# Kernel optimization log

Measured on AMD Instinct MI355X. Metric: run time of the kernel, lower is better.

Reference implementation:

```python
import jax, jax.numpy as jnp
import numpy as np

B, T, C, H = 16, 2048, 1024, 64

def setup_inputs() -> dict:
    key = jax.random.key(0)
    kx, kq, kk, kv = jax.random.split(key, 4)
    x = jax.random.normal(kx, (B, T, C), dtype=jnp.float32)
    Wq = jax.random.normal(kq, (C, H), dtype=jnp.float32) * (C ** -0.5)
    Wk = jax.random.normal(kk, (C, H), dtype=jnp.float32) * (C ** -0.5)
    Wv = jax.random.normal(kv, (C, H), dtype=jnp.float32) * (C ** -0.5)
    return {"x": x, "Wq": Wq, "Wk": Wk, "Wv": Wv}

def reference(x, Wq, Wk, Wv):
    # q,k,v: [B,T,H]
    q = jnp.einsum('btc,ch->bth', x, Wq)
    k = jnp.einsum('btc,ch->bth', x, Wk)
    v = jnp.einsum('btc,ch->bth', x, Wv)
    scale = k.shape[-1] ** -0.5
    # scores: [B,T,T], causal mask then softmax (dropout=0 -> identity)
    w = jnp.einsum('bth,bsh->bts', q, k) * scale
    causal = jnp.tril(jnp.ones((x.shape[1], x.shape[1]), dtype=bool))
    w = jnp.where(causal[None, :, :], w, -jnp.inf)
    w = jax.nn.softmax(w, axis=-1)
    out = jnp.einsum('bts,bsh->bth', w, v)
    return out
```

## Files before the change

kernel.cpp:

```cpp
#include <hip/hip_runtime.h>


#define B_ 16
#define T_ 2048
#define C_ 1024
#define H_ 64
#define QK_ELEMS (B_ * T_ * H_)

typedef float  f32x4  __attribute__((ext_vector_type(4)));
typedef __bf16 bf16x8 __attribute__((ext_vector_type(8)));
typedef __bf16 bf16x4 __attribute__((ext_vector_type(4)));

__global__ __launch_bounds__(256) void wt_kernel(const float* __restrict__ Wq,
                                                 const float* __restrict__ Wk,
                                                 const float* __restrict__ Wv,
                                                 __bf16* __restrict__ Wt) {
    __shared__ float tl[64][65];
    const int mat = blockIdx.x >> 4;
    const int c0  = (blockIdx.x & 15) * 64;
    const float* W = (mat == 0) ? Wq : (mat == 1) ? Wk : Wv;
    const int t  = threadIdx.x;
    const int r4 = t >> 6;
    const int cc = t & 63;
#pragma unroll
    for (int i = 0; i < 16; i++) {
        const int c = r4 + i * 4;
        tl[c][cc] = W[(size_t)(c0 + c) * H_ + cc];
    }
    __syncthreads();
#pragma unroll
    for (int i = 0; i < 16; i++) {
        const int h = r4 + i * 4;
        Wt[(size_t)mat * 65536 + (size_t)h * C_ + c0 + cc] = (__bf16)tl[cc][h];
    }
}

__global__ __launch_bounds__(256) void qkv_kernel(const float* __restrict__ x,
                                                  const __bf16* __restrict__ Wt,
                                                  __bf16* __restrict__ Qw,
                                                  __bf16* __restrict__ Kw,
                                                  __bf16* __restrict__ Vtw) {
    __shared__ __align__(16) __bf16 Alds[2][64 * 72];
    __shared__ __align__(16) __bf16 Blds[2][192 * 72];

    const int tid  = threadIdx.x;
    const int w    = tid >> 6;
    const int lane = tid & 63;
    const int quad = lane >> 4;
    const int l15  = lane & 15;
    const int wm   = (w & 1) * 32;
    const int wn   = (w >> 1) * 96;
    const int m0   = blockIdx.x * 64;

    f32x4 acc[12];
#pragma unroll
    for (int i = 0; i < 12; i++) acc[i] = (f32x4){0.f, 0.f, 0.f, 0.f};

    const int ar = tid >> 3;
    const int ac = (tid & 7) * 8;
    const float* xA = x + (size_t)(m0 + ar) * C_ + ac;
    const __bf16* wB = Wt + (size_t)ar * C_ + ac;

    float4 a0, a1, a2, a3;
    bf16x8 br[6];

    auto loadA = [&](int k0) {
        a0 = *(const float4*)(xA + k0);
        a1 = *(const float4*)(xA + k0 + 4);
        a2 = *(const float4*)(xA + k0 + 32 * C_);
        a3 = *(const float4*)(xA + k0 + 32 * C_ + 4);
    };
    auto loadB = [&](int k0) {
#pragma unroll
        for (int i = 0; i < 6; i++)
            br[i] = *(const bf16x8*)(wB + (size_t)i * 32 * C_ + k0);
    };
    auto storeLds = [&](int buf) {
        bf16x8 v0, v1;
        v0[0]=(__bf16)a0.x; v0[1]=(__bf16)a0.y; v0[2]=(__bf16)a0.z; v0[3]=(__bf16)a0.w;
        v0[4]=(__bf16)a1.x; v0[5]=(__bf16)a1.y; v0[6]=(__bf16)a1.z; v0[7]=(__bf16)a1.w;
        v1[0]=(__bf16)a2.x; v1[1]=(__bf16)a2.y; v1[2]=(__bf16)a2.z; v1[3]=(__bf16)a2.w;
        v1[4]=(__bf16)a3.x; v1[5]=(__bf16)a3.y; v1[6]=(__bf16)a3.z; v1[7]=(__bf16)a3.w;
        *(bf16x8*)&Alds[buf][ar * 72 + ac]        = v0;
        *(bf16x8*)&Alds[buf][(ar + 32) * 72 + ac] = v1;
#pragma unroll
        for (int i = 0; i < 6; i++)
            *(bf16x8*)&Blds[buf][(ar + i * 32) * 72 + ac] = br[i];
    };

    loadA(0); loadB(0); storeLds(0);

    for (int k = 0; k < 16; k++) {
        __syncthreads();
        if (k < 15) { loadA((k + 1) * 64); loadB((k + 1) * 64); }
        const int buf = k & 1;
#pragma unroll
        for (int kh = 0; kh < 2; kh++) {
            bf16x8 af0 = *(const bf16x8*)&Alds[buf][(wm + l15) * 72 + kh * 32 + quad * 8];
            bf16x8 af1 = *(const bf16x8*)&Alds[buf][(wm + 16 + l15) * 72 + kh * 32 + quad * 8];
#pragma unroll
            for (int nt = 0; nt < 6; nt++) {
                bf16x8 bf = *(const bf16x8*)&Blds[buf][(wn + nt * 16 + l15) * 72 + kh * 32 + quad * 8];
                acc[nt]     = __builtin_amdgcn_mfma_f32_16x16x32_bf16(af0, bf, acc[nt], 0, 0, 0);
                acc[6 + nt] = __builtin_amdgcn_mfma_f32_16x16x32_bf16(af1, bf, acc[6 + nt], 0, 0, 0);
            }
        }
        if (k < 15) storeLds((k + 1) & 1);
    }

#pragma unroll
    for (int mt = 0; mt < 2; mt++) {
        const int row0 = m0 + wm + mt * 16 + quad * 4;
#pragma unroll
        for (int nt = 0; nt < 6; nt++) {
            const int col = wn + nt * 16 + l15;
            const int mat = col >> 6;
            const int h   = col & 63;
            const f32x4 a = acc[mt * 6 + nt];
            if (mat == 0) {
#pragma unroll
                for (int r = 0; r < 4; r++)
                    Qw[(size_t)(row0 + r) * H_ + h] = (__bf16)a[r];
            } else if (mat == 1) {
#pragma unroll
                for (int r = 0; r < 4; r++)
                    Kw[(size_t)(row0 + r) * H_ + h] = (__bf16)a[r];
            } else {
                const int bb = row0 >> 11, tt = row0 & 2047;
                bf16x4 pv;
                pv[0]=(__bf16)a[0]; pv[1]=(__bf16)a[1]; pv[2]=(__bf16)a[2]; pv[3]=(__bf16)a[3];
                *(bf16x4*)(Vtw + (((size_t)(bb * H_ + h)) << 11) + tt) = pv;
            }
        }
    }
}

#define SCALE_LOG2E 0.18033688011112042f

__global__ __launch_bounds__(256) void attn_kernel(const __bf16* __restrict__ Qw,
                                                   const __bf16* __restrict__ Kw,
                                                   const __bf16* __restrict__ Vtw,
                                                   float* __restrict__ out) {
    __shared__ __align__(16) __bf16 Klds[2][64 * 72];
    __shared__ __align__(16) __bf16 Vlds[2][64 * 72];
    __shared__ __align__(16) __bf16 Plds[4][16 * 72];

    const int tid  = threadIdx.x;
    const int w    = tid >> 6;
    const int lane = tid & 63;
    const int quad = lane >> 4;
    const int l15  = lane & 15;

    const int b   = blockIdx.x & 15;
    const int qi  = 31 - (blockIdx.x >> 4);
    const int tq0 = qi * 64;
    const size_t bT = (size_t)b * T_;

    const __bf16* qp = Qw + (bT + tq0 + w * 16 + l15) * H_ + quad * 8;
    const bf16x8 qf0 = *(const bf16x8*)qp;
    const bf16x8 qf1 = *(const bf16x8*)(qp + 32);

    float l_acc = 0.f;
    f32x4 accO[4];
#pragma unroll
    for (int nt = 0; nt < 4; nt++) accO[nt] = (f32x4){0.f, 0.f, 0.f, 0.f};

    const int sr = tid >> 3;
    const int sc = (tid & 7) * 8;
    const __bf16* Kbase = Kw + (bT + sr) * H_ + sc;
    const __bf16* Vbase = Vtw + (((size_t)(b * H_ + sr)) << 11) + sc;

    bf16x8 kr0, kr1, vr0, vr1;
    auto loadTile = [&](int ts0) {
        kr0 = *(const bf16x8*)(Kbase + (size_t)ts0 * H_);
        kr1 = *(const bf16x8*)(Kbase + (size_t)(ts0 + 32) * H_);
        vr0 = *(const bf16x8*)(Vbase + ts0);
        vr1 = *(const bf16x8*)(Vbase + ts0 + ((size_t)32 << 11));
    };
    auto storeTile = [&](int buf) {
        *(bf16x8*)&Klds[buf][sr * 72 + sc]        = kr0;
        *(bf16x8*)&Klds[buf][(sr + 32) * 72 + sc] = kr1;
        *(bf16x8*)&Vlds[buf][sr * 72 + sc]        = vr0;
        *(bf16x8*)&Vlds[buf][(sr + 32) * 72 + sc] = vr1;
    };

    loadTile(0); storeTile(0);

    for (int j = 0; j <= qi; j++) {
        __syncthreads();
        if (j < qi) loadTile((j + 1) * 64);
        const int buf = j & 1;

        f32x4 s[4];
#pragma unroll
        for (int nt = 0; nt < 4; nt++) {
            const __bf16* kb = &Klds[buf][(nt * 16 + l15) * 72];
            bf16x8 kf0 = *(const bf16x8*)(kb + quad * 8);
            bf16x8 kf1 = *(const bf16x8*)(kb + 32 + quad * 8);
            f32x4 z = (f32x4){0.f, 0.f, 0.f, 0.f};
            z     = __builtin_amdgcn_mfma_f32_16x16x32_bf16(kf0, qf0, z, 0, 0, 0);
            s[nt] = __builtin_amdgcn_mfma_f32_16x16x32_bf16(kf1, qf1, z, 0, 0, 0);
        }

        float p[4][4];
        if (j == qi) {
            const int ts0 = j * 64;
            const int qg  = tq0 + w * 16 + l15;
#pragma unroll
            for (int nt = 0; nt < 4; nt++)
#pragma unroll
                for (int r = 0; r < 4; r++) {
                    const int key = ts0 + nt * 16 + quad * 4 + r;
                    float e = exp2f(__builtin_fmaf(s[nt][r], SCALE_LOG2E, -8.0f));
                    e = (key > qg) ? 0.f : e;
                    p[nt][r] = e;
                    l_acc += e;
                }
        } else {
#pragma unroll
            for (int nt = 0; nt < 4; nt++)
#pragma unroll
                for (int r = 0; r < 4; r++) {
                    float e = exp2f(__builtin_fmaf(s[nt][r], SCALE_LOG2E, -8.0f));
                    p[nt][r] = e;
                    l_acc += e;
                }
        }

        __bf16* pw = &Plds[w][l15 * 72 + quad * 4];
#pragma unroll
        for (int nt = 0; nt < 4; nt++) {
            bf16x4 pv;
            pv[0]=(__bf16)p[nt][0]; pv[1]=(__bf16)p[nt][1];
            pv[2]=(__bf16)p[nt][2]; pv[3]=(__bf16)p[nt][3];
            *(bf16x4*)(pw + nt * 16) = pv;
        }
        __asm__ __volatile__("s_waitcnt lgkmcnt(0)" ::: "memory");

        const __bf16* pr = &Plds[w][l15 * 72];
        bf16x8 pf0 = *(const bf16x8*)(pr + quad * 8);
        bf16x8 pf1 = *(const bf16x8*)(pr + 32 + quad * 8);
#pragma unroll
        for (int nt = 0; nt < 4; nt++) {
            const __bf16* vb = &Vlds[buf][(nt * 16 + l15) * 72];
            bf16x8 vf0 = *(const bf16x8*)(vb + quad * 8);
            bf16x8 vf1 = *(const bf16x8*)(vb + 32 + quad * 8);
            accO[nt] = __builtin_amdgcn_mfma_f32_16x16x32_bf16(pf0, vf0, accO[nt], 0, 0, 0);
            accO[nt] = __builtin_amdgcn_mfma_f32_16x16x32_bf16(pf1, vf1, accO[nt], 0, 0, 0);
        }
        if (j < qi) storeTile((j + 1) & 1);
    }

    l_acc += __shfl_xor(l_acc, 16);
    l_acc += __shfl_xor(l_acc, 32);

    const size_t orow0 = (bT + tq0 + w * 16 + quad * 4) * H_;
#pragma unroll
    for (int r = 0; r < 4; r++) {
        const float linv = 1.0f / __shfl(l_acc, quad * 4 + r);
#pragma unroll
        for (int nt = 0; nt < 4; nt++)
            out[orow0 + (size_t)r * H_ + nt * 16 + l15] = accO[nt][r] * linv;
    }
}

extern "C" void kernel_launch(void* const* d_in, const int* in_sizes, int n_in,
                              void* d_out, int out_size, void* d_ws, size_t ws_size,
                              hipStream_t stream) {
    const float* x  = (const float*)d_in[0];
    const float* Wq = (const float*)d_in[1];
    const float* Wk = (const float*)d_in[2];
    const float* Wv = (const float*)d_in[3];
    float* out = (float*)d_out;

    __bf16* Qw  = (__bf16*)d_ws;
    __bf16* Kw  = Qw + QK_ELEMS;
    __bf16* Vtw = Kw + QK_ELEMS;
    __bf16* Wt  = Vtw + QK_ELEMS;

    wt_kernel<<<dim3(48), dim3(256), 0, stream>>>(Wq, Wk, Wv, Wt);
    qkv_kernel<<<dim3((B_ * T_) / 64), dim3(256), 0, stream>>>(x, Wt, Qw, Kw, Vtw);
    attn_kernel<<<dim3(B_ * 32), dim3(256), 0, stream>>>(Qw, Kw, Vtw, out);
}
```

Baseline: 248.4 us.

## Split attention KV range into chunks with reduction; async swizzled B loads; staged V transpose

The attention kernel is split along the key dimension into up to four chunks of eight tiles per query block, which raises the grid from 512 to 1280 blocks. A new reduce kernel sums the partial outputs and row sums and normalises them. This works because the softmax uses no running max, so partial sums add directly. The QKV projection now loads the weight tile with global_load_lds into an XOR-swizzled unpadded LDS layout, and it writes the transposed V through LDS as coalesced 16-byte stores. The cost is an extra kernel launch and partial-result traffic through global memory.

```diff
diff --git a/kernel.cpp b/kernel.cpp
--- a/kernel.cpp
+++ b/kernel.cpp
@@ -10,6 +10,12 @@
 typedef float  f32x4  __attribute__((ext_vector_type(4)));
 typedef __bf16 bf16x8 __attribute__((ext_vector_type(8)));
 typedef __bf16 bf16x4 __attribute__((ext_vector_type(4)));
+
+__device__ __forceinline__ void glds16(const void* g, void* l) {
+    __builtin_amdgcn_global_load_lds(
+        (const __attribute__((address_space(1))) void*)g,
+        (__attribute__((address_space(3))) void*)l, 16, 0, 0);
+}
 
 __global__ __launch_bounds__(256) void wt_kernel(const float* __restrict__ Wq,
                                                  const float* __restrict__ Wk,
@@ -31,7 +37,8 @@
 #pragma unroll
     for (int i = 0; i < 16; i++) {
         const int h = r4 + i * 4;
-        Wt[(size_t)mat * 65536 + (size_t)h * C_ + c0 + cc] = (__bf16)tl[cc][h];
+        const int cc2 = ((((cc >> 3) ^ (h & 7)) << 3) | (cc & 7));
+        Wt[(size_t)mat * 65536 + (size_t)h * C_ + c0 + cc2] = (__bf16)tl[cc][h];
     }
 }
 
@@ -41,7 +48,7 @@
                                                   __bf16* __restrict__ Kw,
                                                   __bf16* __restrict__ Vtw) {
     __shared__ __align__(16) __bf16 Alds[2][64 * 72];
-    __shared__ __align__(16) __bf16 Blds[2][192 * 72];
+    __shared__ __align__(16) __bf16 Blds[2][192 * 64];
 
     const int tid  = threadIdx.x;
     const int w    = tid >> 6;
@@ -59,23 +66,16 @@
     const int ar = tid >> 3;
     const int ac = (tid & 7) * 8;
     const float* xA = x + (size_t)(m0 + ar) * C_ + ac;
-    const __bf16* wB = Wt + (size_t)ar * C_ + ac;
+    const __bf16* bsrc = Wt + (size_t)(w * 48 + (lane >> 3)) * C_ + (lane & 7) * 8;
 
     float4 a0, a1, a2, a3;
-    bf16x8 br[6];
-
     auto loadA = [&](int k0) {
         a0 = *(const float4*)(xA + k0);
         a1 = *(const float4*)(xA + k0 + 4);
         a2 = *(const float4*)(xA + k0 + 32 * C_);
         a3 = *(const float4*)(xA + k0 + 32 * C_ + 4);
     };
-    auto loadB = [&](int k0) {
-#pragma unroll
-        for (int i = 0; i < 6; i++)
-            br[i] = *(const bf16x8*)(wB + (size_t)i * 32 * C_ + k0);
-    };
-    auto storeLds = [&](int buf) {
+    auto storeA = [&](int buf) {
         bf16x8 v0, v1;
         v0[0]=(__bf16)a0.x; v0[1]=(__bf16)a0.y; v0[2]=(__bf16)a0.z; v0[3]=(__bf16)a0.w;
         v0[4]=(__bf16)a1.x; v0[5]=(__bf16)a1.y; v0[6]=(__bf16)a1.z; v0[7]=(__bf16)a1.w;
@@ -83,29 +83,35 @@
         v1[4]=(__bf16)a3.x; v1[5]=(__bf16)a3.y; v1[6]=(__bf16)a3.z; v1[7]=(__bf16)a3.w;
         *(bf16x8*)&Alds[buf][ar * 72 + ac]        = v0;
         *(bf16x8*)&Alds[buf][(ar + 32) * 72 + ac] = v1;
+    };
+    auto asyncB = [&](int k0, int buf) {
+        __bf16* dst = &Blds[buf][(w * 48) * 64];
+        const __bf16* src = bsrc + k0;
 #pragma unroll
         for (int i = 0; i < 6; i++)
-            *(bf16x8*)&Blds[buf][(ar + i * 32) * 72 + ac] = br[i];
-    };
-
-    loadA(0); loadB(0); storeLds(0);
+            glds16(src + (size_t)i * 8 * C_, dst + i * 8 * 64);
+    };
+
+    asyncB(0, 0); loadA(0); storeA(0);
 
     for (int k = 0; k < 16; k++) {
         __syncthreads();
-        if (k < 15) { loadA((k + 1) * 64); loadB((k + 1) * 64); }
+        const int kn = k + 1;
+        if (kn < 16) { asyncB(kn * 64, kn & 1); loadA(kn * 64); }
         const int buf = k & 1;
 #pragma unroll
         for (int kh = 0; kh < 2; kh++) {
             bf16x8 af0 = *(const bf16x8*)&Alds[buf][(wm + l15) * 72 + kh * 32 + quad * 8];
             bf16x8 af1 = *(const bf16x8*)&Alds[buf][(wm + 16 + l15) * 72 + kh * 32 + quad * 8];
+            const int ch8 = ((((kh << 2) + quad) ^ (l15 & 7)) << 3);
 #pragma unroll
             for (int nt = 0; nt < 6; nt++) {
-                bf16x8 bf = *(const bf16x8*)&Blds[buf][(wn + nt * 16 + l15) * 72 + kh * 32 + quad * 8];
-                acc[nt]     = __builtin_amdgcn_mfma_f32_16x16x32_bf16(af0, bf, acc[nt], 0, 0, 0);
-                acc[6 + nt] = __builtin_amdgcn_mfma_f32_16x16x32_bf16(af1, bf, acc[6 + nt], 0, 0, 0);
+                bf16x8 bfr = *(const bf16x8*)&Blds[buf][(wn + nt * 16 + l15) * 64 + ch8];
+                acc[nt]     = __builtin_amdgcn_mfma_f32_16x16x32_bf16(af0, bfr, acc[nt], 0, 0, 0);
+                acc[6 + nt] = __builtin_amdgcn_mfma_f32_16x16x32_bf16(af1, bfr, acc[6 + nt], 0, 0, 0);
             }
         }
-        if (k < 15) storeLds((k + 1) & 1);
+        if (kn < 16) storeA(kn & 1);
     }
 
 #pragma unroll
@@ -114,23 +120,43 @@
 #pragma unroll
         for (int nt = 0; nt < 6; nt++) {
             const int col = wn + nt * 16 + l15;
-            const int mat = col >> 6;
-            const int h   = col & 63;
             const f32x4 a = acc[mt * 6 + nt];
-            if (mat == 0) {
+            if (wn + nt * 16 < 64) {
 #pragma unroll
                 for (int r = 0; r < 4; r++)
-                    Qw[(size_t)(row0 + r) * H_ + h] = (__bf16)a[r];
-            } else if (mat == 1) {
+                    Qw[(size_t)(row0 + r) * H_ + col] = (__bf16)a[r];
+            } else if (wn + nt * 16 < 128) {
 #pragma unroll
                 for (int r = 0; r < 4; r++)
-                    Kw[(size_t)(row0 + r) * H_ + h] = (__bf16)a[r];
-            } else {
-                const int bb = row0 >> 11, tt = row0 & 2047;
+                    Kw[(size_t)(row0 + r) * H_ + col - 64] = (__bf16)a[r];
+            }
+        }
+    }
+    __bf16* Vt_l = &Alds[0][0];
+    if (w >= 2) {
+#pragma unroll
+        for (int mt = 0; mt < 2; mt++) {
+            const int t0 = wm + mt * 16 + quad * 4;
+#pragma unroll
+            for (int nt = 2; nt < 6; nt++) {
+                const int h = (nt - 2) * 16 + l15;
+                const f32x4 a = acc[mt * 6 + nt];
                 bf16x4 pv;
                 pv[0]=(__bf16)a[0]; pv[1]=(__bf16)a[1]; pv[2]=(__bf16)a[2]; pv[3]=(__bf16)a[3];
-                *(bf16x4*)(Vtw + (((size_t)(bb * H_ + h)) << 11) + tt) = pv;
+                *(bf16x4*)&Vt_l[h * 72 + t0] = pv;
             }
+        }
+    }
+    __syncthreads();
+    if (w >= 2) {
+        const int bb   = m0 >> 11;
+        const int tblk = m0 & 2047;
+#pragma unroll
+        for (int i = 0; i < 4; i++) {
+            const int hh = (w - 2) * 32 + i * 8 + (lane >> 3);
+            const int tt = (lane & 7) * 8;
+            *(bf16x8*)(Vtw + (((size_t)(bb * H_ + hh)) << 11) + tblk + tt) =
+                *(const bf16x8*)&Vt_l[hh * 72 + tt];
         }
     }
 }
@@ -140,7 +166,8 @@
 __global__ __launch_bounds__(256) void attn_kernel(const __bf16* __restrict__ Qw,
                                                    const __bf16* __restrict__ Kw,
                                                    const __bf16* __restrict__ Vtw,
-                                                   float* __restrict__ out) {
+                                                   float* __restrict__ Opart,
+                                                   float* __restrict__ Lpart) {
     __shared__ __align__(16) __bf16 Klds[2][64 * 72];
     __shared__ __align__(16) __bf16 Vlds[2][64 * 72];
     __shared__ __align__(16) __bf16 Plds[4][16 * 72];
@@ -152,7 +179,16 @@
     const int l15  = lane & 15;
 
     const int b   = blockIdx.x & 15;
-    const int qi  = 31 - (blockIdx.x >> 4);
+    const int cid = 79 - (blockIdx.x >> 4);
+    int qi, ci;
+    if (cid < 8)       { qi = cid;                  ci = 0; }
+    else if (cid < 24) { qi = 8 + ((cid - 8) >> 1); ci = (cid - 8) & 1; }
+    else if (cid < 48) { const int u = cid - 24; const int d = u / 3;
+                         qi = 16 + d;               ci = u - d * 3; }
+    else               { qi = 24 + ((cid - 48) >> 2); ci = (cid - 48) & 3; }
+    const int j0 = ci * 8;
+    const int j1 = (j0 + 8 < qi + 1) ? j0 + 8 : qi + 1;
+    const int nj = j1 - j0;
     const int tq0 = qi * 64;
     const size_t bT = (size_t)b * T_;
 
@@ -184,12 +220,13 @@
         *(bf16x8*)&Vlds[buf][(sr + 32) * 72 + sc] = vr1;
     };
 
-    loadTile(0); storeTile(0);
-
-    for (int j = 0; j <= qi; j++) {
+    loadTile(j0 * 64); storeTile(0);
+
+    for (int jj = 0; jj < nj; jj++) {
+        const int j = j0 + jj;
         __syncthreads();
-        if (j < qi) loadTile((j + 1) * 64);
-        const int buf = j & 1;
+        if (jj + 1 < nj) loadTile((j + 1) * 64);
+        const int buf = jj & 1;
 
         f32x4 s[4];
 #pragma unroll
@@ -248,19 +285,49 @@
             accO[nt] = __builtin_amdgcn_mfma_f32_16x16x32_bf16(pf0, vf0, accO[nt], 0, 0, 0);
             accO[nt] = __builtin_amdgcn_mfma_f32_16x16x32_bf16(pf1, vf1, accO[nt], 0, 0, 0);
         }
-        if (j < qi) storeTile((j + 1) & 1);
+        if (jj + 1 < nj) storeTile((jj + 1) & 1);
     }
 
     l_acc += __shfl_xor(l_acc, 16);
     l_acc += __shfl_xor(l_acc, 32);
 
-    const size_t orow0 = (bT + tq0 + w * 16 + quad * 4) * H_;
-#pragma unroll
-    for (int r = 0; r < 4; r++) {
-        const float linv = 1.0f / __shfl(l_acc, quad * 4 + r);
-#pragma unroll
-        for (int nt = 0; nt < 4; nt++)
-            out[orow0 + (size_t)r * H_ + nt * 16 + l15] = accO[nt][r] * linv;
+    const int slot = (((b << 5) + qi) << 2) + ci;
+    float* Op = Opart + (size_t)slot * 4096;
+#pragma unroll
+    for (int nt = 0; nt < 4; nt++)
+#pragma unroll
+        for (int r = 0; r < 4; r++)
+            Op[(w * 16 + quad * 4 + r) * 64 + nt * 16 + l15] = accO[nt][r];
+    if (quad == 0) Lpart[slot * 64 + w * 16 + l15] = l_acc;
+}
+
+__global__ __launch_bounds__(256) void reduce_kernel(const float* __restrict__ Opart,
+                                                     const float* __restrict__ Lpart,
+                                                     float* __restrict__ out) {
+    const int b  = blockIdx.x & 15;
+    const int qi = blockIdx.x >> 4;
+    const int nc = (qi >> 3) + 1;
+    const int tid = threadIdx.x;
+    const int q  = tid >> 2;
+    const int hc = (tid & 3) * 16;
+    const int sbase = ((b << 5) + qi) << 2;
+
+    f32x4 s[4];
+#pragma unroll
+    for (int i = 0; i < 4; i++) s[i] = (f32x4){0.f, 0.f, 0.f, 0.f};
+    float l = 0.f;
+    for (int ci = 0; ci < nc; ci++) {
+        const float* Op = Opart + (size_t)(sbase + ci) * 4096 + q * 64 + hc;
+#pragma unroll
+        for (int i = 0; i < 4; i++) s[i] += *(const f32x4*)(Op + i * 4);
+        l += Lpart[(sbase + ci) * 64 + q];
+    }
+    const float inv = 1.f / l;
+    float* o = out + ((size_t)b * T_ + qi * 64 + q) * H_ + hc;
+#pragma unroll
+    for (int i = 0; i < 4; i++) {
+        f32x4 r = s[i] * inv;
+        *(f32x4*)(o + i * 4) = r;
     }
 }
 
@@ -277,8 +344,11 @@
     __bf16* Kw  = Qw + QK_ELEMS;
     __bf16* Vtw = Kw + QK_ELEMS;
     __bf16* Wt  = Vtw + QK_ELEMS;
+    float* Opart = (float*)((char*)d_ws + 16777216);
+    float* Lpart = Opart + (size_t)2048 * 4096;
 
     wt_kernel<<<dim3(48), dim3(256), 0, stream>>>(Wq, Wk, Wv, Wt);
     qkv_kernel<<<dim3((B_ * T_) / 64), dim3(256), 0, stream>>>(x, Wt, Qw, Kw, Vtw);
-    attn_kernel<<<dim3(B_ * 32), dim3(256), 0, stream>>>(Qw, Kw, Vtw, out);
-}
+    attn_kernel<<<dim3(1280), dim3(256), 0, stream>>>(Qw, Kw, Vtw, Opart, Lpart);
+    reduce_kernel<<<dim3(512), dim3(256), 0, stream>>>(Opart, Lpart, out);
+}
```

After: 244.2 us. Within noise of the previous version (-1.7%).
